# Optimization experiments

Measured on AMD Instinct MI355X. Metric: run time of the kernel, lower is better.

Reference implementation:

```python
import jax, jax.numpy as jnp
import numpy as np

D_MODEL = 768
NUM_HEADS = 12
D_K = D_MODEL // NUM_HEADS
B, S = 2, 4096


def setup_inputs() -> dict:
    key = jax.random.key(0)
    ks = jax.random.split(key, 11)
    std = 1.0 / np.sqrt(D_MODEL)
    mk = lambda k: (jax.random.normal(k, (D_MODEL, D_MODEL), jnp.float32) * std)
    return {
        "query": jax.random.normal(ks[0], (B, S, D_MODEL), jnp.float32),
        "key": jax.random.normal(ks[1], (B, S, D_MODEL), jnp.float32),
        "value": jax.random.normal(ks[2], (B, S, D_MODEL), jnp.float32),
        "Wq": mk(ks[3]), "bq": jnp.zeros((D_MODEL,), jnp.float32),
        "Wk": mk(ks[4]), "bk": jnp.zeros((D_MODEL,), jnp.float32),
        "Wv": mk(ks[5]), "bv": jnp.zeros((D_MODEL,), jnp.float32),
        "Wo": mk(ks[6]), "bo": jnp.zeros((D_MODEL,), jnp.float32),
    }


def _split_heads(x):
    # [B,S,D] -> [B,H,S,d_k]
    b, s, _ = x.shape
    return x.reshape(b, s, NUM_HEADS, D_K).transpose(0, 2, 1, 3)


def reference(query, key, value, Wq, bq, Wk, bk, Wv, bv, Wo, bo):
    q = _split_heads(query @ Wq.T + bq)
    k = _split_heads(key @ Wk.T + bk)
    v = _split_heads(value @ Wv.T + bv)
    scores = jnp.einsum("bhqd,bhkd->bhqk", q, k) / jnp.sqrt(jnp.float32(D_K))
    attn = jax.nn.softmax(scores, axis=-1)  # dropout is identity in eval
    out = jnp.einsum("bhqk,bhkd->bhqd", attn, v)
    out = out.transpose(0, 2, 1, 3).reshape(query.shape[0], -1, D_MODEL)
    return out @ Wo.T + bo
```

## Files before the change

### kernel.cpp

```cpp
#include <hip/hip_runtime.h>
#include <cstdint>

#define D_MODEL 768
#define NHEAD 12
#define DK 64
#define BATCH 2
#define SEQ 4096
#define MTOT (BATCH * SEQ)
#define NT (SEQ / 64)
#define WSZ (D_MODEL * D_MODEL)

typedef __attribute__((ext_vector_type(8))) _Float16 f16x8;
typedef __attribute__((ext_vector_type(4))) float f32x4;
typedef unsigned short ushort_t;
typedef unsigned int uint_t;

#define SCALE_LOG2E 0.18033688011112042f
#define EXP2(d, s) asm("v_exp_f32 %0, %1" : "=v"(d) : "v"(s))

__device__ __forceinline__ int swz(int row, int col_e) {
    return (row * 128 + col_e * 2) ^ ((row & 7) << 4);
}

__device__ __forceinline__ uint_t pkrtz(float a, float b) {
    return __builtin_bit_cast(uint_t, __builtin_amdgcn_cvt_pkrtz(a, b));
}

__device__ __forceinline__ void gl_lds16(const ushort_t* g, char* l) {
    __builtin_amdgcn_global_load_lds((const __attribute__((address_space(1))) void*)g,
                                     (__attribute__((address_space(3))) void*)l, 16, 0, 0);
}

__global__ __launch_bounds__(256) void cvt7(const float* s0, const float* s1, const float* s2,
                                            const float* s3, const float* s4, const float* s5,
                                            const float* s6, ushort_t* d0, ushort_t* d1,
                                            ushort_t* d2, ushort_t* d3, ushort_t* d4,
                                            ushort_t* d5, ushort_t* d6) {
    const int t = blockIdx.y;
    const float* src;
    ushort_t* dst;
    int n;
    if (t == 0) { src = s0; dst = d0; n = MTOT * D_MODEL; }
    else if (t == 1) { src = s1; dst = d1; n = MTOT * D_MODEL; }
    else if (t == 2) { src = s2; dst = d2; n = MTOT * D_MODEL; }
    else if (t == 3) { src = s3; dst = d3; n = WSZ; }
    else if (t == 4) { src = s4; dst = d4; n = WSZ; }
    else if (t == 5) { src = s5; dst = d5; n = WSZ; }
    else { src = s6; dst = d6; n = WSZ; }
    const int i = (blockIdx.x * 256 + threadIdx.x) * 8;
    if (i >= n) return;
    float4 a = *(const float4*)(src + i);
    float4 b = *(const float4*)(src + i + 4);
    f16x8 h;
    h[0] = (_Float16)a.x; h[1] = (_Float16)a.y; h[2] = (_Float16)a.z; h[3] = (_Float16)a.w;
    h[4] = (_Float16)b.x; h[5] = (_Float16)b.y; h[6] = (_Float16)b.z; h[7] = (_Float16)b.w;
    *(f16x8*)(dst + i) = h;
}

__device__ __forceinline__ void stage_gemm(const ushort_t* __restrict__ Ap,
                                           const ushort_t* __restrict__ Wp,
                                           int m0, int n0, int k0, char* ldsbuf,
                                           int w, int lane) {
    const int r8 = lane >> 3;
    const int cole = (((lane & 7) * 16) ^ (r8 << 4)) >> 1;
#pragma unroll
    for (int j = 0; j < 4; ++j)
        gl_lds16(Ap + (size_t)(m0 + w * 32 + j * 8 + r8) * D_MODEL + k0 + cole,
                 ldsbuf + w * 4096 + j * 1024);
#pragma unroll
    for (int j = 0; j < 2; ++j)
        gl_lds16(Wp + (size_t)(n0 + w * 16 + j * 8 + r8) * D_MODEL + k0 + cole,
                 ldsbuf + 16384 + w * 2048 + j * 1024);
}

template <int MODE>
__global__ __launch_bounds__(256) void gemm_f16(const ushort_t* __restrict__ Ap,
                                                const ushort_t* __restrict__ Wp,
                                                const float* __restrict__ bias,
                                                void* __restrict__ Cp,
                                                float alpha) {
    __shared__ __align__(16) char lds[49152];
    const int tid = threadIdx.x;
    const int lane = tid & 63;
    const int w = tid >> 6;
    const int li = lane & 15;
    const int g = lane >> 4;
    const int wr = w >> 1, wc = w & 1;
    const int m0 = blockIdx.y * 128;
    const int n0 = blockIdx.x * 64;

    f32x4 acc[4][2];
#pragma unroll
    for (int fr = 0; fr < 4; ++fr)
#pragma unroll
        for (int fc = 0; fc < 2; ++fc) acc[fr][fc] = (f32x4){0.f, 0.f, 0.f, 0.f};

    stage_gemm(Ap, Wp, m0, n0, 0, lds, w, lane);
    __syncthreads();

    for (int kk = 0; kk < 6; ++kk) {
#pragma unroll
        for (int ph = 0; ph < 2; ++ph) {
            const int it = kk * 2 + ph;
            char* cur = lds + (ph ? 24576 : 0);
            if (it + 1 < 12)
                stage_gemm(Ap, Wp, m0, n0, (it + 1) * 64, lds + (ph ? 0 : 24576), w, lane);
#pragma unroll
            for (int ks = 0; ks < 2; ++ks) {
                f16x8 ar[4], br[2];
#pragma unroll
                for (int fr = 0; fr < 4; ++fr)
                    ar[fr] = *(const f16x8*)(cur + swz(wr * 64 + fr * 16 + li, ks * 32 + g * 8));
#pragma unroll
                for (int fc = 0; fc < 2; ++fc)
                    br[fc] = *(const f16x8*)(cur + 16384 + swz(wc * 32 + fc * 16 + li, ks * 32 + g * 8));
#pragma unroll
                for (int fr = 0; fr < 4; ++fr)
#pragma unroll
                    for (int fc = 0; fc < 2; ++fc)
                        acc[fr][fc] = __builtin_amdgcn_mfma_f32_16x16x32_f16(ar[fr], br[fc], acc[fr][fc], 0, 0, 0);
            }
            if (it + 1 < 12) __syncthreads();
        }
    }

#pragma unroll
    for (int fr = 0; fr < 4; ++fr)
#pragma unroll
        for (int fc = 0; fc < 2; ++fc)
#pragma unroll
            for (int r = 0; r < 4; ++r) {
                const int m = m0 + wr * 64 + fr * 16 + g * 4 + r;
                const int d = wc * 32 + fc * 16 + li;
                float val = acc[fr][fc][r] + bias[n0 + d];
                if (MODE == 0) {
                    ((float*)Cp)[(size_t)m * D_MODEL + n0 + d] = val;
                } else {
                    val *= alpha;
                    const int b = m >> 12;
                    const int s = m & (SEQ - 1);
                    const size_t idx = (((size_t)b * NHEAD + blockIdx.x) * SEQ + s) * DK + d;
                    ((ushort_t*)Cp)[idx] = __builtin_bit_cast(ushort_t, (_Float16)val);
                }
            }
}

__global__ __launch_bounds__(512, 4) void flash5(const ushort_t* __restrict__ q_g,
                                                 const ushort_t* __restrict__ k_g,
                                                 const ushort_t* __restrict__ v_g,
                                                 ushort_t* __restrict__ aw) {
    __shared__ __align__(16) char lds[49152];

    const int tid = threadIdx.x;
    const int lane = tid & 63;
    const int w = tid >> 6;
    const int li = lane & 15;
    const int g = lane >> 4;
    const int bh = blockIdx.y;
    const int q0 = blockIdx.x * 128;

    const ushort_t* qp = q_g + (size_t)bh * SEQ * DK;
    const ushort_t* kp = k_g + (size_t)bh * SEQ * DK;
    const ushort_t* vp = v_g + (size_t)bh * SEQ * DK;

    f16x8 qf[2];
#pragma unroll
    for (int ks = 0; ks < 2; ++ks)
        qf[ks] = *(const f16x8*)(qp + (size_t)(q0 + w * 16 + li) * DK + ks * 32 + g * 8);

    const int kr8 = lane >> 3;
    const int kcole = (((lane & 7) * 16) ^ (kr8 << 4)) >> 1;
    const ushort_t* ksrc = kp + (size_t)(w * 8 + kr8) * DK + kcole;
    char* const kdst0 = lds + 0 + w * 1024;
    char* const kdst1 = lds + 8192 + w * 1024;

    const int vd = lane;
    const ushort_t* vsrc = vp + (size_t)(w * 8) * DK + vd;
    const int vw0 = swz(vd, w * 8);
    const int vw1 = swz(vd, w * 8 + 4);

    gl_lds16(ksrc, kdst0);
    ushort_t vr[8];
#pragma unroll
    for (int j = 0; j < 8; ++j) vr[j] = vsrc[(size_t)j * DK];
    {
        ushort4 u0, u1;
        u0.x = vr[0]; u0.y = vr[1]; u0.z = vr[2]; u0.w = vr[3];
        u1.x = vr[4]; u1.y = vr[5]; u1.z = vr[6]; u1.w = vr[7];
        *(ushort4*)(lds + 16384 + vw0) = u0;
        *(ushort4*)(lds + 16384 + vw1) = u1;
    }
    __syncthreads();

    f32x4 oacc[4];
#pragma unroll
    for (int i = 0; i < 4; ++i) oacc[i] = (f32x4){0.f, 0.f, 0.f, 0.f};
    float m_r = -1e30f, l_r = 0.f;

    const int pb = 32768 + w * 2048;

    for (int kt2 = 0; kt2 < NT / 2; ++kt2) {
#pragma unroll
        for (int ph = 0; ph < 2; ++ph) {
            const int kt = kt2 * 2 + ph;
            const int KBc = ph ? 8192 : 0;
            const int VBc = ph ? 24576 : 16384;
            const int VBn = ph ? 16384 : 24576;
            const bool pre = (kt + 1 < NT);

            if (pre) {
                gl_lds16(ksrc + (size_t)(kt + 1) * 64 * DK, ph ? kdst0 : kdst1);
#pragma unroll
                for (int j = 0; j < 8; ++j)
                    vr[j] = vsrc[((size_t)(kt + 1) * 64 + j) * DK];
            }

            f32x4 sacc[4];
#pragma unroll
            for (int t = 0; t < 4; ++t) {
                sacc[t] = (f32x4){0.f, 0.f, 0.f, 0.f};
#pragma unroll
                for (int ks = 0; ks < 2; ++ks) {
                    f16x8 kf = *(const f16x8*)(lds + KBc + swz(t * 16 + li, ks * 32 + g * 8));
                    sacc[t] = __builtin_amdgcn_mfma_f32_16x16x32_f16(kf, qf[ks], sacc[t], 0, 0, 0);
                }
            }

            float t0 = fmaxf(fmaxf(sacc[0][0], sacc[0][1]), fmaxf(sacc[0][2], sacc[0][3]));
            float t1 = fmaxf(fmaxf(sacc[1][0], sacc[1][1]), fmaxf(sacc[1][2], sacc[1][3]));
            float t2 = fmaxf(fmaxf(sacc[2][0], sacc[2][1]), fmaxf(sacc[2][2], sacc[2][3]));
            float t3 = fmaxf(fmaxf(sacc[3][0], sacc[3][1]), fmaxf(sacc[3][2], sacc[3][3]));
            float mx = fmaxf(fmaxf(t0, t1), fmaxf(t2, t3));
            mx = fmaxf(mx, __shfl_xor(mx, 16));
            mx = fmaxf(mx, __shfl_xor(mx, 32));

            if (__any(mx > m_r + 8.0f)) {
                const float nm = fmaxf(m_r, mx);
                float corr;
                float dd = m_r - nm;
                EXP2(corr, dd);
                m_r = nm;
                l_r *= corr;
#pragma unroll
                for (int dt = 0; dt < 4; ++dt) oacc[dt] *= corr;
            }

#pragma unroll
            for (int t = 0; t < 4; ++t) {
                float p0, p1, p2, p3;
                float e0 = sacc[t][0] - m_r;
                float e1 = sacc[t][1] - m_r;
                float e2 = sacc[t][2] - m_r;
                float e3 = sacc[t][3] - m_r;
                EXP2(p0, e0); EXP2(p1, e1); EXP2(p2, e2); EXP2(p3, e3);
                l_r += (p0 + p1) + (p2 + p3);
                uint2 pk;
                pk.x = pkrtz(p0, p1);
                pk.y = pkrtz(p2, p3);
                *(uint2*)(lds + pb + swz(li, t * 16 + g * 4)) = pk;
            }

            f16x8 pbf[2];
#pragma unroll
            for (int ks = 0; ks < 2; ++ks)
                pbf[ks] = *(const f16x8*)(lds + pb + swz(li, ks * 32 + g * 8));
#pragma unroll
            for (int dt = 0; dt < 4; ++dt)
#pragma unroll
                for (int ks = 0; ks < 2; ++ks) {
                    f16x8 vf = *(const f16x8*)(lds + VBc + swz(dt * 16 + li, ks * 32 + g * 8));
                    oacc[dt] = __builtin_amdgcn_mfma_f32_16x16x32_f16(vf, pbf[ks], oacc[dt], 0, 0, 0);
                }

            if (pre) {
                ushort4 u0, u1;
                u0.x = vr[0]; u0.y = vr[1]; u0.z = vr[2]; u0.w = vr[3];
                u1.x = vr[4]; u1.y = vr[5]; u1.z = vr[6]; u1.w = vr[7];
                *(ushort4*)(lds + VBn + vw0) = u0;
                *(ushort4*)(lds + VBn + vw1) = u1;
                __syncthreads();
            }
        }
    }

    float lt = l_r;
    lt += __shfl_xor(lt, 16);
    lt += __shfl_xor(lt, 32);
    const float inv = 1.0f / lt;
    const int b = bh / NHEAD;
    const int hh = bh % NHEAD;
    const int qrow = q0 + w * 16 + li;
#pragma unroll
    for (int dt = 0; dt < 4; ++dt) {
        uint2 o;
        o.x = pkrtz(oacc[dt][0] * inv, oacc[dt][1] * inv);
        o.y = pkrtz(oacc[dt][2] * inv, oacc[dt][3] * inv);
        *(uint2*)&aw[((size_t)b * SEQ + qrow) * D_MODEL + hh * DK + dt * 16 + g * 4] = o;
    }
}

extern "C" void kernel_launch(void* const* d_in, const int* in_sizes, int n_in,
                              void* d_out, int out_size, void* d_ws, size_t ws_size,
                              hipStream_t stream) {
    const float* q_in = (const float*)d_in[0];
    const float* k_in = (const float*)d_in[1];
    const float* v_in = (const float*)d_in[2];
    const float* Wq = (const float*)d_in[3];
    const float* bq = (const float*)d_in[4];
    const float* Wk = (const float*)d_in[5];
    const float* bk = (const float*)d_in[6];
    const float* Wv = (const float*)d_in[7];
    const float* bv = (const float*)d_in[8];
    const float* Wo = (const float*)d_in[9];
    const float* bo = (const float*)d_in[10];
    float* out = (float*)d_out;

    const size_t per = (size_t)MTOT * D_MODEL;
    ushort_t* x16q = (ushort_t*)d_ws;
    ushort_t* x16k = x16q + per;
    ushort_t* x16v = x16k + per;
    ushort_t* w16 = x16v + per;
    ushort_t* qh = w16 + 4 * (size_t)WSZ;
    ushort_t* kh = qh + per;
    ushort_t* vh = kh + per;
    ushort_t* aw = vh + per;

    dim3 blk(256);
    dim3 gcvt(MTOT * D_MODEL / (256 * 8), 7);
    hipLaunchKernelGGL(cvt7, gcvt, blk, 0, stream, q_in, k_in, v_in, Wq, Wk, Wv, Wo,
                       x16q, x16k, x16v, w16, w16 + WSZ, w16 + 2 * WSZ, w16 + 3 * WSZ);

    dim3 gproj(D_MODEL / 64, MTOT / 128);
    hipLaunchKernelGGL((gemm_f16<1>), gproj, blk, 0, stream, x16q, w16, bq, qh, SCALE_LOG2E);
    hipLaunchKernelGGL((gemm_f16<1>), gproj, blk, 0, stream, x16k, w16 + WSZ, bk, kh, 1.0f);
    hipLaunchKernelGGL((gemm_f16<1>), gproj, blk, 0, stream, x16v, w16 + 2 * WSZ, bv, vh, 1.0f);

    dim3 gattn(SEQ / 128, BATCH * NHEAD);
    hipLaunchKernelGGL(flash5, gattn, dim3(512), 0, stream, qh, kh, vh, aw);

    hipLaunchKernelGGL((gemm_f16<0>), gproj, blk, 0, stream, aw, w16 + 3 * WSZ, bo, out, 1.0f);
}
```

Before: 374.6 us.

## Give each flash wave two query tiles, halve block size, remap GEMM blocks

The attention kernel now runs 4 waves of 256 threads, each handling 32 query rows as two 16-row halves. Each K and V fragment read from LDS is reused for two MFMAs, which halves LDS reads per FLOP, and s_setprio is raised around the MFMA sections. The GEMM kernel remaps block indices with an XCD-style swizzle so neighbouring blocks share A/W tiles in cache. The cost is more registers per wave and more staging work per thread, which could lower occupancy.

```diff
diff --git a/kernel.cpp b/kernel.cpp
--- a/kernel.cpp
+++ b/kernel.cpp
@@ -86,8 +86,11 @@
     const int li = lane & 15;
     const int g = lane >> 4;
     const int wr = w >> 1, wc = w & 1;
-    const int m0 = blockIdx.y * 128;
-    const int n0 = blockIdx.x * 64;
+    const int lin = blockIdx.x + 12 * blockIdx.y;
+    const int sw = (lin & 7) * 96 + (lin >> 3);
+    const int nx = sw % 12;
+    const int m0 = (sw / 12) * 128;
+    const int n0 = nx * 64;
 
     f32x4 acc[4][2];
 #pragma unroll
@@ -139,17 +142,17 @@
                     val *= alpha;
                     const int b = m >> 12;
                     const int s = m & (SEQ - 1);
-                    const size_t idx = (((size_t)b * NHEAD + blockIdx.x) * SEQ + s) * DK + d;
+                    const size_t idx = (((size_t)b * NHEAD + nx) * SEQ + s) * DK + d;
                     ((ushort_t*)Cp)[idx] = __builtin_bit_cast(ushort_t, (_Float16)val);
                 }
             }
 }
 
-__global__ __launch_bounds__(512, 4) void flash5(const ushort_t* __restrict__ q_g,
+__global__ __launch_bounds__(256, 4) void flash6(const ushort_t* __restrict__ q_g,
                                                  const ushort_t* __restrict__ k_g,
                                                  const ushort_t* __restrict__ v_g,
                                                  ushort_t* __restrict__ aw) {
-    __shared__ __align__(16) char lds[49152];
+    __shared__ __align__(16) char lds[40960];
 
     const int tid = threadIdx.x;
     const int lane = tid & 63;
@@ -163,39 +166,47 @@
     const ushort_t* kp = k_g + (size_t)bh * SEQ * DK;
     const ushort_t* vp = v_g + (size_t)bh * SEQ * DK;
 
-    f16x8 qf[2];
-#pragma unroll
-    for (int ks = 0; ks < 2; ++ks)
-        qf[ks] = *(const f16x8*)(qp + (size_t)(q0 + w * 16 + li) * DK + ks * 32 + g * 8);
+    f16x8 qf[2][2];
+#pragma unroll
+    for (int h = 0; h < 2; ++h)
+#pragma unroll
+        for (int ks = 0; ks < 2; ++ks)
+            qf[h][ks] = *(const f16x8*)(qp + (size_t)(q0 + w * 32 + h * 16 + li) * DK + ks * 32 + g * 8);
 
     const int kr8 = lane >> 3;
     const int kcole = (((lane & 7) * 16) ^ (kr8 << 4)) >> 1;
-    const ushort_t* ksrc = kp + (size_t)(w * 8 + kr8) * DK + kcole;
-    char* const kdst0 = lds + 0 + w * 1024;
-    char* const kdst1 = lds + 8192 + w * 1024;
-
+    const ushort_t* ksrc = kp + (size_t)(w * 16 + kr8) * DK + kcole;
     const int vd = lane;
-    const ushort_t* vsrc = vp + (size_t)(w * 8) * DK + vd;
-    const int vw0 = swz(vd, w * 8);
-    const int vw1 = swz(vd, w * 8 + 4);
-
-    gl_lds16(ksrc, kdst0);
-    ushort_t vr[8];
-#pragma unroll
-    for (int j = 0; j < 8; ++j) vr[j] = vsrc[(size_t)j * DK];
+    const ushort_t* vsrc = vp + (size_t)(w * 16) * DK + vd;
+    const int vw0 = swz(vd, w * 16);
+    const int vw1 = swz(vd, w * 16 + 4);
+    const int vw2 = swz(vd, w * 16 + 8);
+    const int vw3 = swz(vd, w * 16 + 12);
+
+    gl_lds16(ksrc, lds + 0 + w * 2048);
+    gl_lds16(ksrc + 8 * DK, lds + 0 + w * 2048 + 1024);
+    ushort_t vr[16];
+#pragma unroll
+    for (int j = 0; j < 16; ++j) vr[j] = vsrc[(size_t)j * DK];
     {
-        ushort4 u0, u1;
-        u0.x = vr[0]; u0.y = vr[1]; u0.z = vr[2]; u0.w = vr[3];
-        u1.x = vr[4]; u1.y = vr[5]; u1.z = vr[6]; u1.w = vr[7];
-        *(ushort4*)(lds + 16384 + vw0) = u0;
-        *(ushort4*)(lds + 16384 + vw1) = u1;
+        ushort4 u;
+        u.x = vr[0]; u.y = vr[1]; u.z = vr[2]; u.w = vr[3];
+        *(ushort4*)(lds + 16384 + vw0) = u;
+        u.x = vr[4]; u.y = vr[5]; u.z = vr[6]; u.w = vr[7];
+        *(ushort4*)(lds + 16384 + vw1) = u;
+        u.x = vr[8]; u.y = vr[9]; u.z = vr[10]; u.w = vr[11];
+        *(ushort4*)(lds + 16384 + vw2) = u;
+        u.x = vr[12]; u.y = vr[13]; u.z = vr[14]; u.w = vr[15];
+        *(ushort4*)(lds + 16384 + vw3) = u;
     }
     __syncthreads();
 
-    f32x4 oacc[4];
-#pragma unroll
-    for (int i = 0; i < 4; ++i) oacc[i] = (f32x4){0.f, 0.f, 0.f, 0.f};
-    float m_r = -1e30f, l_r = 0.f;
+    f32x4 oacc[2][4];
+#pragma unroll
+    for (int h = 0; h < 2; ++h)
+#pragma unroll
+        for (int i = 0; i < 4; ++i) oacc[h][i] = (f32x4){0.f, 0.f, 0.f, 0.f};
+    float m_r[2] = {-1e30f, -1e30f}, l_r[2] = {0.f, 0.f};
 
     const int pb = 32768 + w * 2048;
 
@@ -204,98 +215,125 @@
         for (int ph = 0; ph < 2; ++ph) {
             const int kt = kt2 * 2 + ph;
             const int KBc = ph ? 8192 : 0;
+            const int KBn = ph ? 0 : 8192;
             const int VBc = ph ? 24576 : 16384;
             const int VBn = ph ? 16384 : 24576;
             const bool pre = (kt + 1 < NT);
 
             if (pre) {
-                gl_lds16(ksrc + (size_t)(kt + 1) * 64 * DK, ph ? kdst0 : kdst1);
-#pragma unroll
-                for (int j = 0; j < 8; ++j)
+                gl_lds16(ksrc + (size_t)(kt + 1) * 64 * DK, lds + KBn + w * 2048);
+                gl_lds16(ksrc + (size_t)((kt + 1) * 64 + 8) * DK, lds + KBn + w * 2048 + 1024);
+#pragma unroll
+                for (int j = 0; j < 16; ++j)
                     vr[j] = vsrc[((size_t)(kt + 1) * 64 + j) * DK];
             }
 
-            f32x4 sacc[4];
-#pragma unroll
-            for (int t = 0; t < 4; ++t) {
-                sacc[t] = (f32x4){0.f, 0.f, 0.f, 0.f};
+            f32x4 sacc[2][4];
+#pragma unroll
+            for (int h = 0; h < 2; ++h)
+#pragma unroll
+                for (int t = 0; t < 4; ++t) sacc[h][t] = (f32x4){0.f, 0.f, 0.f, 0.f};
+            __builtin_amdgcn_s_setprio(1);
+#pragma unroll
+            for (int t = 0; t < 4; ++t)
 #pragma unroll
                 for (int ks = 0; ks < 2; ++ks) {
                     f16x8 kf = *(const f16x8*)(lds + KBc + swz(t * 16 + li, ks * 32 + g * 8));
-                    sacc[t] = __builtin_amdgcn_mfma_f32_16x16x32_f16(kf, qf[ks], sacc[t], 0, 0, 0);
-                }
-            }
-
-            float t0 = fmaxf(fmaxf(sacc[0][0], sacc[0][1]), fmaxf(sacc[0][2], sacc[0][3]));
-            float t1 = fmaxf(fmaxf(sacc[1][0], sacc[1][1]), fmaxf(sacc[1][2], sacc[1][3]));
-            float t2 = fmaxf(fmaxf(sacc[2][0], sacc[2][1]), fmaxf(sacc[2][2], sacc[2][3]));
-            float t3 = fmaxf(fmaxf(sacc[3][0], sacc[3][1]), fmaxf(sacc[3][2], sacc[3][3]));
-            float mx = fmaxf(fmaxf(t0, t1), fmaxf(t2, t3));
-            mx = fmaxf(mx, __shfl_xor(mx, 16));
-            mx = fmaxf(mx, __shfl_xor(mx, 32));
-
-            if (__any(mx > m_r + 8.0f)) {
-                const float nm = fmaxf(m_r, mx);
-                float corr;
-                float dd = m_r - nm;
-                EXP2(corr, dd);
-                m_r = nm;
-                l_r *= corr;
-#pragma unroll
-                for (int dt = 0; dt < 4; ++dt) oacc[dt] *= corr;
-            }
-
-#pragma unroll
-            for (int t = 0; t < 4; ++t) {
-                float p0, p1, p2, p3;
-                float e0 = sacc[t][0] - m_r;
-                float e1 = sacc[t][1] - m_r;
-                float e2 = sacc[t][2] - m_r;
-                float e3 = sacc[t][3] - m_r;
-                EXP2(p0, e0); EXP2(p1, e1); EXP2(p2, e2); EXP2(p3, e3);
-                l_r += (p0 + p1) + (p2 + p3);
-                uint2 pk;
-                pk.x = pkrtz(p0, p1);
-                pk.y = pkrtz(p2, p3);
-                *(uint2*)(lds + pb + swz(li, t * 16 + g * 4)) = pk;
-            }
-
-            f16x8 pbf[2];
-#pragma unroll
-            for (int ks = 0; ks < 2; ++ks)
-                pbf[ks] = *(const f16x8*)(lds + pb + swz(li, ks * 32 + g * 8));
+                    sacc[0][t] = __builtin_amdgcn_mfma_f32_16x16x32_f16(kf, qf[0][ks], sacc[0][t], 0, 0, 0);
+                    sacc[1][t] = __builtin_amdgcn_mfma_f32_16x16x32_f16(kf, qf[1][ks], sacc[1][t], 0, 0, 0);
+                }
+            __builtin_amdgcn_s_setprio(0);
+
+            float mx[2];
+#pragma unroll
+            for (int h = 0; h < 2; ++h) {
+                float t0 = fmaxf(fmaxf(sacc[h][0][0], sacc[h][0][1]), fmaxf(sacc[h][0][2], sacc[h][0][3]));
+                float t1 = fmaxf(fmaxf(sacc[h][1][0], sacc[h][1][1]), fmaxf(sacc[h][1][2], sacc[h][1][3]));
+                float t2 = fmaxf(fmaxf(sacc[h][2][0], sacc[h][2][1]), fmaxf(sacc[h][2][2], sacc[h][2][3]));
+                float t3 = fmaxf(fmaxf(sacc[h][3][0], sacc[h][3][1]), fmaxf(sacc[h][3][2], sacc[h][3][3]));
+                float m = fmaxf(fmaxf(t0, t1), fmaxf(t2, t3));
+                m = fmaxf(m, __shfl_xor(m, 16));
+                m = fmaxf(m, __shfl_xor(m, 32));
+                mx[h] = m;
+            }
+            if (__any((mx[0] > m_r[0] + 8.0f) || (mx[1] > m_r[1] + 8.0f))) {
+#pragma unroll
+                for (int h = 0; h < 2; ++h) {
+                    const float nm = fmaxf(m_r[h], mx[h]);
+                    float corr;
+                    float dd = m_r[h] - nm;
+                    EXP2(corr, dd);
+                    m_r[h] = nm;
+                    l_r[h] *= corr;
+#pragma unroll
+                    for (int dt = 0; dt < 4; ++dt) oacc[h][dt] *= corr;
+                }
+            }
+
+            f16x8 pbf[2][2];
+#pragma unroll
+            for (int h = 0; h < 2; ++h) {
+#pragma unroll
+                for (int t = 0; t < 4; ++t) {
+                    float p0, p1, p2, p3;
+                    float e0 = sacc[h][t][0] - m_r[h];
+                    float e1 = sacc[h][t][1] - m_r[h];
+                    float e2 = sacc[h][t][2] - m_r[h];
+                    float e3 = sacc[h][t][3] - m_r[h];
+                    EXP2(p0, e0); EXP2(p1, e1); EXP2(p2, e2); EXP2(p3, e3);
+                    l_r[h] += (p0 + p1) + (p2 + p3);
+                    uint2 pk;
+                    pk.x = pkrtz(p0, p1);
+                    pk.y = pkrtz(p2, p3);
+                    *(uint2*)(lds + pb + swz(li, t * 16 + g * 4)) = pk;
+                }
+#pragma unroll
+                for (int ks = 0; ks < 2; ++ks)
+                    pbf[h][ks] = *(const f16x8*)(lds + pb + swz(li, ks * 32 + g * 8));
+            }
+
+            __builtin_amdgcn_s_setprio(1);
 #pragma unroll
             for (int dt = 0; dt < 4; ++dt)
 #pragma unroll
                 for (int ks = 0; ks < 2; ++ks) {
                     f16x8 vf = *(const f16x8*)(lds + VBc + swz(dt * 16 + li, ks * 32 + g * 8));
-                    oacc[dt] = __builtin_amdgcn_mfma_f32_16x16x32_f16(vf, pbf[ks], oacc[dt], 0, 0, 0);
-                }
+                    oacc[0][dt] = __builtin_amdgcn_mfma_f32_16x16x32_f16(vf, pbf[0][ks], oacc[0][dt], 0, 0, 0);
+                    oacc[1][dt] = __builtin_amdgcn_mfma_f32_16x16x32_f16(vf, pbf[1][ks], oacc[1][dt], 0, 0, 0);
+                }
+            __builtin_amdgcn_s_setprio(0);
 
             if (pre) {
-                ushort4 u0, u1;
-                u0.x = vr[0]; u0.y = vr[1]; u0.z = vr[2]; u0.w = vr[3];
-                u1.x = vr[4]; u1.y = vr[5]; u1.z = vr[6]; u1.w = vr[7];
-                *(ushort4*)(lds + VBn + vw0) = u0;
-                *(ushort4*)(lds + VBn + vw1) = u1;
+                ushort4 u;
+                u.x = vr[0]; u.y = vr[1]; u.z = vr[2]; u.w = vr[3];
+                *(ushort4*)(lds + VBn + vw0) = u;
+                u.x = vr[4]; u.y = vr[5]; u.z = vr[6]; u.w = vr[7];
+                *(ushort4*)(lds + VBn + vw1) = u;
+                u.x = vr[8]; u.y = vr[9]; u.z = vr[10]; u.w = vr[11];
+                *(ushort4*)(lds + VBn + vw2) = u;
+                u.x = vr[12]; u.y = vr[13]; u.z = vr[14]; u.w = vr[15];
+                *(ushort4*)(lds + VBn + vw3) = u;
                 __syncthreads();
             }
         }
     }
 
-    float lt = l_r;
-    lt += __shfl_xor(lt, 16);
-    lt += __shfl_xor(lt, 32);
-    const float inv = 1.0f / lt;
     const int b = bh / NHEAD;
     const int hh = bh % NHEAD;
-    const int qrow = q0 + w * 16 + li;
-#pragma unroll
-    for (int dt = 0; dt < 4; ++dt) {
-        uint2 o;
-        o.x = pkrtz(oacc[dt][0] * inv, oacc[dt][1] * inv);
-        o.y = pkrtz(oacc[dt][2] * inv, oacc[dt][3] * inv);
-        *(uint2*)&aw[((size_t)b * SEQ + qrow) * D_MODEL + hh * DK + dt * 16 + g * 4] = o;
+#pragma unroll
+    for (int h = 0; h < 2; ++h) {
+        float lt = l_r[h];
+        lt += __shfl_xor(lt, 16);
+        lt += __shfl_xor(lt, 32);
+        const float inv = 1.0f / lt;
+        const int qrow = q0 + w * 32 + h * 16 + li;
+#pragma unroll
+        for (int dt = 0; dt < 4; ++dt) {
+            uint2 o;
+            o.x = pkrtz(oacc[h][dt][0] * inv, oacc[h][dt][1] * inv);
+            o.y = pkrtz(oacc[h][dt][2] * inv, oacc[h][dt][3] * inv);
+            *(uint2*)&aw[((size_t)b * SEQ + qrow) * D_MODEL + hh * DK + dt * 16 + g * 4] = o;
+        }
     }
 }
 
@@ -336,7 +374,7 @@
     hipLaunchKernelGGL((gemm_f16<1>), gproj, blk, 0, stream, x16v, w16 + 2 * WSZ, bv, vh, 1.0f);
 
     dim3 gattn(SEQ / 128, BATCH * NHEAD);
-    hipLaunchKernelGGL(flash5, gattn, dim3(512), 0, stream, qh, kh, vh, aw);
+    hipLaunchKernelGGL(flash6, gattn, blk, 0, stream, qh, kh, vh, aw);
 
     hipLaunchKernelGGL((gemm_f16<0>), gproj, blk, 0, stream, aw, w16 + 3 * WSZ, bo, out, 1.0f);
 }
```

After: 430.3 us. 1.15x slower.
